# Kernel optimization log

Measured on AMD Instinct MI355X. Metric: run time of the kernel, lower is better.

The kernel has to match this reference:

```python
import jax, jax.numpy as jnp
import numpy as np

N = 20000      # total nodes across the mini-batch of graphs
E = 320000     # edges (avg degree 16)
B = 16         # graphs in the batch
HEADS = 8
EPS_BN = 1e-5
NEG_SLOPE = 0.2


def _lin(k, fan_in, fan_out):
    return (jax.random.normal(k, (fan_in, fan_out), jnp.float32) / np.float32(np.sqrt(fan_in)))


def setup_inputs() -> dict:
    key = jax.random.key(0)
    ks = jax.random.split(key, 24)
    inp = {}
    inp["x"] = jax.random.normal(ks[0], (N, 3), jnp.float32)
    inp["edge_index"] = jax.random.randint(ks[1], (2, E), 0, N, dtype=jnp.int32)
    inp["batch"] = jnp.sort(jax.random.randint(ks[2], (N,), 0, B, dtype=jnp.int32))
    # GATConv params: lin weight [in, heads*out], att_src/att_dst [heads,out], bias [heads*out]
    dims = [(3, 16), (128, 32), (256, 64)]
    for i, (cin, cout) in enumerate(dims, start=1):
        base = 3 + 5 * i
        inp[f"W{i}"] = _lin(ks[base], cin, HEADS * cout)
        inp[f"as{i}"] = jax.random.normal(ks[base + 1], (HEADS, cout), jnp.float32) * 0.1
        inp[f"ad{i}"] = jax.random.normal(ks[base + 2], (HEADS, cout), jnp.float32) * 0.1
        inp[f"b{i}"] = jnp.zeros((HEADS * cout,), jnp.float32)
        inp[f"g{i}"] = jnp.ones((HEADS * cout,), jnp.float32)
        inp[f"be{i}"] = jnp.zeros((HEADS * cout,), jnp.float32)
    inp["fcW"] = _lin(ks[20], 512, 10)
    inp["fcb"] = jnp.zeros((10,), jnp.float32)
    return inp


def gat_layer(x, src, dst, W, a_s, a_d, bias, heads, out_ch):
    n = x.shape[0]
    h = (x @ W).reshape(n, heads, out_ch)              # [N,H,C]
    al_s = jnp.einsum('nhc,hc->nh', h, a_s)            # [N,H]
    al_d = jnp.einsum('nhc,hc->nh', h, a_d)
    e = jax.nn.leaky_relu(al_s[src] + al_d[dst], NEG_SLOPE)   # [E,H]
    m = jax.ops.segment_max(e, dst, num_segments=n)    # per-dst softmax (stable)
    e = jnp.exp(e - m[dst])
    denom = jax.ops.segment_sum(e, dst, num_segments=n)
    alpha = e / (denom[dst] + 1e-16)
    out = jax.ops.segment_sum(h[src] * alpha[:, :, None], dst, num_segments=n)
    return out.reshape(n, heads * out_ch) + bias


def bn_relu(x, g, b):
    mu = x.mean(0)
    var = x.var(0)  # biased, as torch BN uses for normalization
    return jax.nn.relu((x - mu) * jax.lax.rsqrt(var + EPS_BN) * g + b)


def reference(x, edge_index, batch, W1, as1, ad1, b1, g1, be1,
              W2, as2, ad2, b2, g2, be2, W3, as3, ad3, b3, g3, be3, fcW, fcb):
    n = x.shape[0]
    loops = jnp.arange(n, dtype=edge_index.dtype)
    src = jnp.concatenate([edge_index[0], loops])  # add_self_loops=True (PyG default)
    dst = jnp.concatenate([edge_index[1], loops])
    h = bn_relu(gat_layer(x, src, dst, W1, as1, ad1, b1, HEADS, 16), g1, be1)
    h = bn_relu(gat_layer(h, src, dst, W2, as2, ad2, b2, HEADS, 32), g2, be2)
    h = bn_relu(gat_layer(h, src, dst, W3, as3, ad3, b3, HEADS, 64), g3, be3)
    pooled = jax.ops.segment_max(h, batch, num_segments=B)  # global_max_pool
    return pooled @ fcW + fcb
```

## Files before the change

### kernel.cpp

```cpp
#include <hip/hip_runtime.h>
#include <hip/hip_bf16.h>

#define HEADS 8
#define EPS_BN 1e-5f
#define NEG_SLOPE 0.2f
#define BN_NB 256
#define PAD 96

typedef __attribute__((ext_vector_type(8))) short bf16x8;
typedef __attribute__((ext_vector_type(4))) float f32x4;

__device__ __forceinline__ float bf2f(unsigned short u) {
    return __uint_as_float(((unsigned int)u) << 16);
}

__device__ __forceinline__ unsigned short f2bf(float f) {
    __hip_bfloat16 b = __float2bfloat16(f);
    return *reinterpret_cast<unsigned short*>(&b);
}

__device__ __forceinline__ void gld_lds16(const ushort* g, ushort* l) {
    __builtin_amdgcn_global_load_lds(
        (const __attribute__((address_space(1))) unsigned int*)g,
        (__attribute__((address_space(3))) unsigned int*)l, 16, 0, 0);
}


__global__ void scatter_pad_kernel(const int* __restrict__ ei, int E, int N,
                                   int* __restrict__ counts, int* __restrict__ csr_pad) {
    int i = blockIdx.x * blockDim.x + threadIdx.x;
    int total = E + N;
    if (i >= total) return;
    int s, d;
    if (i < E) { s = ei[i]; d = ei[E + i]; } else { s = i - E; d = i - E; }
    int slot = atomicAdd(&counts[d], 1);
    if (slot < PAD) csr_pad[d * PAD + slot] = s;
}


__global__ __launch_bounds__(256) void linear1_al_tr_kernel(const float* __restrict__ x,
                                                            const float* __restrict__ W,
                                                            const float* __restrict__ a_s,
                                                            const float* __restrict__ a_d,
                                                            ushort* __restrict__ h,
                                                            float* __restrict__ als,
                                                            float* __restrict__ ald, int N,
                                                            const float* __restrict__ W2,
                                                            ushort* __restrict__ Wt2,
                                                            const float* __restrict__ W3,
                                                            ushort* __restrict__ Wt3) {
    __shared__ float t[32][33];
    int tid = threadIdx.x;
    int bid = blockIdx.x;
    if (bid < 160) {
        const float* Ws; ushort* Wt; int K, Nc, b;
        if (bid < 32) { Ws = W2; Wt = Wt2; K = 128; Nc = 256; b = bid; }
        else          { Ws = W3; Wt = Wt3; K = 256; Nc = 512; b = bid - 32; }
        int nb = Nc / 32;
        int bx = b % nb, by = b / nb;
        int n0 = bx * 32, k0 = by * 32;
        int lx = tid & 31, ly = tid >> 5;
        for (int r = ly; r < 32; r += 8) t[r][lx] = Ws[(size_t)(k0 + r) * Nc + n0 + lx];
        __syncthreads();
        for (int r = ly; r < 32; r += 8) Wt[(size_t)(n0 + r) * K + k0 + lx] = f2bf(t[lx][r]);
    }
    int n = bid * 2 + (tid >> 7);
    int f = tid & 127;
    if (n >= N) return;
    float acc = x[n * 3 + 0] * W[f] + x[n * 3 + 1] * W[128 + f] + x[n * 3 + 2] * W[256 + f];
    h[(size_t)n * 128 + f] = f2bf(acc);
    float s = acc * a_s[f];
    float ds = acc * a_d[f];
    s += __shfl_xor(s, 1);  ds += __shfl_xor(ds, 1);
    s += __shfl_xor(s, 2);  ds += __shfl_xor(ds, 2);
    s += __shfl_xor(s, 4);  ds += __shfl_xor(ds, 4);
    s += __shfl_xor(s, 8);  ds += __shfl_xor(ds, 8);
    if ((f & 15) == 0) {
        int head = f >> 4;
        als[n * 8 + head] = s;
        ald[n * 8 + head] = ds;
    }
}


template<int K, int C>
__global__ __launch_bounds__(256) void mfma_gemm_kernel(const ushort* __restrict__ A,
                                                        const float* __restrict__ scale,
                                                        const float* __restrict__ shift,
                                                        const ushort* __restrict__ Bt,
                                                        ushort* __restrict__ Cout,
                                                        const float* __restrict__ a_s,
                                                        const float* __restrict__ a_d,
                                                        float* __restrict__ als,
                                                        float* __restrict__ ald,
                                                        int M, int Ncols) {
    __shared__ __align__(16) ushort lA[128 * 64];
    __shared__ __align__(16) ushort lB[128 * 64];
    __shared__ __align__(16) float s_scale[K];
    __shared__ __align__(16) float s_shift[K];
    int tid = threadIdx.x;
    int l = tid & 63, w = tid >> 6;
    int m0 = blockIdx.x * 128;
    int n0 = blockIdx.y * 128;
    int wm = w >> 1, wn = w & 1;
    for (int i = tid; i < K; i += 256) {
        s_scale[i] = scale[i];
        s_shift[i] = shift[i];
    }
    f32x4 zero = {0.f, 0.f, 0.f, 0.f};
    f32x4 acc[4][4];
#pragma unroll
    for (int m = 0; m < 4; ++m)
#pragma unroll
        for (int n = 0; n < 4; ++n) acc[m][n] = zero;
    __syncthreads();

#pragma unroll
    for (int k0 = 0; k0 < K; k0 += 64) {
        if (k0) __syncthreads();
#pragma unroll
        for (int i = 0; i < 4; ++i) {
            int idx = (w * 4 + i) * 64 + l;
            int row = idx >> 3, p = idx & 7;
            int gc = (p ^ (row & 7)) * 8;
            gld_lds16(Bt + (size_t)(n0 + row) * K + k0 + gc, &lB[idx * 8]);
        }
#pragma unroll
        for (int i = 0; i < 4; ++i) {
            int idx = (w * 4 + i) * 64 + l;
            int row = idx >> 3, p = idx & 7;
            int gc = (p ^ (row & 7)) * 8;
            int ar = m0 + row; ar = (ar < M) ? ar : (M - 1);
            int kk = k0 + gc;
            uint4 raw = *(const uint4*)(A + (size_t)ar * K + kk);
            float4 sc0 = *(const float4*)(s_scale + kk);
            float4 sc1 = *(const float4*)(s_scale + kk + 4);
            float4 sh0 = *(const float4*)(s_shift + kk);
            float4 sh1 = *(const float4*)(s_shift + kk + 4);
            unsigned int rr0 = raw.x, rr1 = raw.y, rr2 = raw.z, rr3 = raw.w;
            float v0, v1;
            unsigned int o0, o1, o2, o3;
            v0 = fmaxf(__uint_as_float(rr0 << 16) * sc0.x + sh0.x, 0.f);
            v1 = fmaxf(__uint_as_float(rr0 & 0xffff0000u) * sc0.y + sh0.y, 0.f);
            o0 = (unsigned int)f2bf(v0) | ((unsigned int)f2bf(v1) << 16);
            v0 = fmaxf(__uint_as_float(rr1 << 16) * sc0.z + sh0.z, 0.f);
            v1 = fmaxf(__uint_as_float(rr1 & 0xffff0000u) * sc0.w + sh0.w, 0.f);
            o1 = (unsigned int)f2bf(v0) | ((unsigned int)f2bf(v1) << 16);
            v0 = fmaxf(__uint_as_float(rr2 << 16) * sc1.x + sh1.x, 0.f);
            v1 = fmaxf(__uint_as_float(rr2 & 0xffff0000u) * sc1.y + sh1.y, 0.f);
            o2 = (unsigned int)f2bf(v0) | ((unsigned int)f2bf(v1) << 16);
            v0 = fmaxf(__uint_as_float(rr3 << 16) * sc1.z + sh1.z, 0.f);
            v1 = fmaxf(__uint_as_float(rr3 & 0xffff0000u) * sc1.w + sh1.w, 0.f);
            o3 = (unsigned int)f2bf(v0) | ((unsigned int)f2bf(v1) << 16);
            uint4 pk = {o0, o1, o2, o3};
            *(uint4*)&lA[idx * 8] = pk;
        }
        __syncthreads();
#pragma unroll
        for (int ks = 0; ks < 2; ++ks) {
            bf16x8 af[4], bfr[4];
#pragma unroll
            for (int m = 0; m < 4; ++m) {
                int row = wm * 64 + m * 16 + (l & 15);
                int cp = (ks * 4 + (l >> 4)) ^ (row & 7);
                af[m] = *(const bf16x8*)&lA[row * 64 + cp * 8];
            }
#pragma unroll
            for (int n = 0; n < 4; ++n) {
                int row = wn * 64 + n * 16 + (l & 15);
                int cp = (ks * 4 + (l >> 4)) ^ (row & 7);
                bfr[n] = *(const bf16x8*)&lB[row * 64 + cp * 8];
            }
#pragma unroll
            for (int m = 0; m < 4; ++m)
#pragma unroll
                for (int n = 0; n < 4; ++n)
                    acc[m][n] = __builtin_amdgcn_mfma_f32_16x16x32_bf16(af[m], bfr[n], acc[m][n], 0, 0, 0);
        }
    }
    int lr = (l >> 4) * 4, lc = l & 15;
#pragma unroll
    for (int m = 0; m < 4; ++m) {
#pragma unroll
        for (int q = 0; q < 4; ++q) {
            int r = m0 + wm * 64 + m * 16 + lr + q;
            if (r < M) {
#pragma unroll
                for (int n = 0; n < 4; ++n) {
                    int c = n0 + wn * 64 + n * 16 + lc;
                    Cout[(size_t)r * Ncols + c] = f2bf(acc[m][n][q]);
                }
            }
        }
    }
    constexpr int GRP = (C == 64) ? 4 : 2;
    constexpr int NGRP = 4 / GRP;
    float asv[4], adv[4];
#pragma unroll
    for (int n = 0; n < 4; ++n) {
        int cc = n0 + wn * 64 + n * 16 + lc;
        asv[n] = a_s[cc];
        adv[n] = a_d[cc];
    }
#pragma unroll
    for (int m = 0; m < 4; ++m) {
#pragma unroll
        for (int q = 0; q < 4; ++q) {
            int r = m0 + wm * 64 + m * 16 + lr + q;
#pragma unroll
            for (int gg = 0; gg < NGRP; ++gg) {
                float s = 0.f, ds = 0.f;
#pragma unroll
                for (int nn = 0; nn < GRP; ++nn) {
                    int n = gg * GRP + nn;
                    s += acc[m][n][q] * asv[n];
                    ds += acc[m][n][q] * adv[n];
                }
                s += __shfl_xor(s, 1);  ds += __shfl_xor(ds, 1);
                s += __shfl_xor(s, 2);  ds += __shfl_xor(ds, 2);
                s += __shfl_xor(s, 4);  ds += __shfl_xor(ds, 4);
                s += __shfl_xor(s, 8);  ds += __shfl_xor(ds, 8);
                if (lc == 0 && r < M) {
                    int head = (n0 + wn * 64 + gg * (GRP * 16)) / C;
                    als[r * 8 + head] = s;
                    ald[r * 8 + head] = ds;
                }
            }
        }
    }
}


template<int CPL>
__device__ __forceinline__ void gather_accum(const ushort* hp, float wt, float* acc) {
    unsigned int u[CPL / 2];
    if constexpr (CPL == 8) {
        uint4 v = *(const uint4*)hp; u[0] = v.x; u[1] = v.y; u[2] = v.z; u[3] = v.w;
    } else if constexpr (CPL == 4) {
        uint2 v = *(const uint2*)hp; u[0] = v.x; u[1] = v.y;
    } else {
        u[0] = *(const unsigned int*)hp;
    }
#pragma unroll
    for (int j = 0; j < CPL / 2; ++j) {
        acc[2 * j]     += wt * __uint_as_float(u[j] << 16);
        acc[2 * j + 1] += wt * __uint_as_float(u[j] & 0xffff0000u);
    }
}

template<int F, int C>
__global__ __launch_bounds__(256) void aggregate_kernel(const ushort* __restrict__ h,
                                                        const float* __restrict__ als,
                                                        const float* __restrict__ ald,
                                                        const int* __restrict__ counts,
                                                        const int* __restrict__ csr_pad,
                                                        const float* __restrict__ bias,
                                                        ushort* __restrict__ outbf, int N) {
    constexpr int CPL = F / 64;
    int w = threadIdx.x >> 6, l = threadIdx.x & 63;
    int d = blockIdx.x * 4 + w;
    if (d >= N) return;
    int start = d * PAD;
    int deg = counts[d];
    deg = (deg < PAD) ? deg : PAD;
    int hf = l >> 3;
    int hw = l & 7;
    int jslot = l >> 3;
    float aldw = ald[d * 8 + hw];

    float acc[CPL];
#pragma unroll
    for (int j = 0; j < CPL; ++j) acc[j] = 0.f;
    float dsum = 0.f;
    float mrun = -1e30f;

    int nfull = deg & ~7;
    for (int eb = 0; eb < nfull; eb += 8) {
        int sE = (l < 8) ? csr_pad[start + eb + l] : 0;
        int smy = __shfl(sE, jslot);
        float v = als[smy * 8 + hw] + aldw;
        v = (v > 0.f) ? v : NEG_SLOPE * v;
        float bm = v;
        bm = fmaxf(bm, __shfl_xor(bm, 8));
        bm = fmaxf(bm, __shfl_xor(bm, 16));
        bm = fmaxf(bm, __shfl_xor(bm, 32));
        float mnew = fmaxf(mrun, bm);
        float rs = __expf(mrun - mnew);
        float pw = __expf(v - mnew);
        dsum = dsum * rs + pw;
        float rsg = __shfl(rs, hf);
#pragma unroll
        for (int j = 0; j < CPL; ++j) acc[j] *= rsg;
        mrun = mnew;
#pragma unroll
        for (int j = 0; j < 8; ++j) {
            int sj = __shfl(sE, j);
            float wt = __shfl(pw, (j << 3) + hf);
            gather_accum<CPL>(h + (size_t)sj * F + l * CPL, wt, acc);
        }
    }
    int rem = deg - nfull;
    if (rem) {
        int sE = (l < rem) ? csr_pad[start + nfull + l] : 0;
        int smy = __shfl(sE, jslot);
        float v = -1e30f;
        if (jslot < rem) {
            v = als[smy * 8 + hw] + aldw;
            v = (v > 0.f) ? v : NEG_SLOPE * v;
        }
        float bm = v;
        bm = fmaxf(bm, __shfl_xor(bm, 8));
        bm = fmaxf(bm, __shfl_xor(bm, 16));
        bm = fmaxf(bm, __shfl_xor(bm, 32));
        float mnew = fmaxf(mrun, bm);
        float rs = __expf(mrun - mnew);
        float pw = __expf(v - mnew);
        dsum = dsum * rs + pw;
        float rsg = __shfl(rs, hf);
#pragma unroll
        for (int j = 0; j < CPL; ++j) acc[j] *= rsg;
        for (int j = 0; j < rem; ++j) {
            int sj = __shfl(sE, j);
            float wt = __shfl(pw, (j << 3) + hf);
            gather_accum<CPL>(h + (size_t)sj * F + l * CPL, wt, acc);
        }
    }
    dsum += __shfl_xor(dsum, 8);
    dsum += __shfl_xor(dsum, 16);
    dsum += __shfl_xor(dsum, 32);
    float den = __shfl(dsum, hf);
    float inv = 1.0f / (den + 1e-16f);
    int cbase = l * CPL;
#pragma unroll
    for (int j = 0; j < CPL; ++j)
        outbf[(size_t)d * F + cbase + j] = f2bf(acc[j] * inv + bias[cbase + j]);
}


template<int F>
__global__ __launch_bounds__(256) void bnA_kernel(const ushort* __restrict__ xb,
                                                  float* __restrict__ part,
                                                  int N, int npb) {
    constexpr int F4 = F / 4;
    constexpr int RPI = 256 / F4;
    __shared__ float sdata[256 * 8];
    int tid = threadIdx.x;
    int c4 = tid % F4;
    int ro = tid / F4;
    int n0 = blockIdx.x * npb;
    int n1 = n0 + npb;
    if (n1 > N) n1 = N;
    float s0 = 0, s1 = 0, s2 = 0, s3 = 0, q0 = 0, q1 = 0, q2 = 0, q3 = 0;
    for (int r = n0 + ro; r < n1; r += RPI) {
        ushort4 u = *(const ushort4*)(xb + (size_t)r * F + c4 * 4);
        float v0 = bf2f(u.x), v1 = bf2f(u.y), v2 = bf2f(u.z), v3 = bf2f(u.w);
        s0 += v0; s1 += v1; s2 += v2; s3 += v3;
        q0 += v0 * v0; q1 += v1 * v1; q2 += v2 * v2; q3 += v3 * v3;
    }
    float* sp = &sdata[tid * 8];
    sp[0] = s0; sp[1] = s1; sp[2] = s2; sp[3] = s3;
    sp[4] = q0; sp[5] = q1; sp[6] = q2; sp[7] = q3;
    __syncthreads();
    if (tid < F4) {
        float t[8];
#pragma unroll
        for (int k = 0; k < 8; ++k) t[k] = sdata[tid * 8 + k];
        for (int j = 1; j < RPI; ++j) {
            const float* op = &sdata[(j * F4 + tid) * 8];
#pragma unroll
            for (int k = 0; k < 8; ++k) t[k] += op[k];
        }
        float* pb = part + (size_t)blockIdx.x * 2 * F;
#pragma unroll
        for (int k = 0; k < 4; ++k) {
            pb[tid * 4 + k]     = t[k];
            pb[F + tid * 4 + k] = t[4 + k];
        }
    }
}

template<int F>
__global__ void bnB_kernel(const float* __restrict__ part,
                           const float* __restrict__ g, const float* __restrict__ be,
                           float* __restrict__ scale, float* __restrict__ shift, int N) {
    int f = blockIdx.x * blockDim.x + threadIdx.x;
    if (f >= F) return;
    float sum = 0.f, sq = 0.f;
#pragma unroll 4
    for (int j = 0; j < BN_NB; ++j) {
        sum += part[(size_t)j * 2 * F + f];
        sq  += part[(size_t)j * 2 * F + F + f];
    }
    float invN = 1.0f / (float)N;
    float mean = sum * invN;
    float var = sq * invN - mean * mean;
    float sc = g[f] * rsqrtf(var + EPS_BN);
    scale[f] = sc;
    shift[f] = be[f] - mean * sc;
}


__global__ __launch_bounds__(256) void poolA_kernel(const ushort* __restrict__ xb,
                                                    const int* __restrict__ batch,
                                                    const float* __restrict__ scale,
                                                    const float* __restrict__ shift,
                                                    float* __restrict__ pooled8, int N) {
    int tid = threadIdx.x;
    int c4 = tid & 127;
    int ro = tid >> 7;
    int n0 = blockIdx.x * 64;
    int n1 = n0 + 64;
    if (n1 > N) n1 = N;
    float4 sc = ((const float4*)scale)[c4];
    float4 sh = ((const float4*)shift)[c4];
    float* pbase = pooled8 + (size_t)(blockIdx.x & 7) * (16 * 512);
    float m0 = 0.f, m1 = 0.f, m2 = 0.f, m3 = 0.f;
    int cur = -1;
    for (int n = n0 + ro; n < n1; n += 2) {
        int b = batch[n];
        if (b != cur) {
            if (cur >= 0) {
                int base = cur * 512 + c4 * 4;
                atomicMax((int*)&pbase[base],     __float_as_int(m0));
                atomicMax((int*)&pbase[base + 1], __float_as_int(m1));
                atomicMax((int*)&pbase[base + 2], __float_as_int(m2));
                atomicMax((int*)&pbase[base + 3], __float_as_int(m3));
            }
            cur = b;
            m0 = m1 = m2 = m3 = 0.f;
        }
        ushort4 u = *(const ushort4*)(xb + (size_t)n * 512 + c4 * 4);
        m0 = fmaxf(m0, bf2f(u.x) * sc.x + sh.x);
        m1 = fmaxf(m1, bf2f(u.y) * sc.y + sh.y);
        m2 = fmaxf(m2, bf2f(u.z) * sc.z + sh.z);
        m3 = fmaxf(m3, bf2f(u.w) * sc.w + sh.w);
    }
    if (cur >= 0) {
        int base = cur * 512 + c4 * 4;
        atomicMax((int*)&pbase[base],     __float_as_int(m0));
        atomicMax((int*)&pbase[base + 1], __float_as_int(m1));
        atomicMax((int*)&pbase[base + 2], __float_as_int(m2));
        atomicMax((int*)&pbase[base + 3], __float_as_int(m3));
    }
}

__global__ __launch_bounds__(512) void poolFC_kernel(const float* __restrict__ pooled8,
                                                     const float* __restrict__ fcW,
                                                     const float* __restrict__ fcb,
                                                     float* __restrict__ out) {
    __shared__ float sp[16 * 513];
    __shared__ float sw[512 * 10];
    int tid = threadIdx.x;
    for (int c = tid; c < 16 * 512; c += 512) {
        float m = pooled8[c];
#pragma unroll
        for (int k = 1; k < 8; ++k) m = fmaxf(m, pooled8[k * 16 * 512 + c]);
        int b = c >> 9, f = c & 511;
        sp[b * 513 + f] = m;
    }
    for (int i = tid; i < 512 * 10; i += 512) sw[i] = fcW[i];
    __syncthreads();
    if (tid < 160) {
        int b = tid / 10, j = tid % 10;
        float acc = fcb[j];
        const float* spb = &sp[b * 513];
#pragma unroll 8
        for (int f = 0; f < 512; ++f) acc += spb[f] * sw[f * 10 + j];
        out[tid] = acc;
    }
}


extern "C" void kernel_launch(void* const* d_in, const int* in_sizes, int n_in,
                              void* d_out, int out_size, void* d_ws, size_t ws_size,
                              hipStream_t stream) {
    const float* x   = (const float*)d_in[0];
    const int* ei    = (const int*)d_in[1];
    const int* batch = (const int*)d_in[2];
    const float* W1  = (const float*)d_in[3];
    const float* as1 = (const float*)d_in[4];
    const float* ad1 = (const float*)d_in[5];
    const float* b1  = (const float*)d_in[6];
    const float* g1  = (const float*)d_in[7];
    const float* be1 = (const float*)d_in[8];
    const float* W2  = (const float*)d_in[9];
    const float* as2 = (const float*)d_in[10];
    const float* ad2 = (const float*)d_in[11];
    const float* b2  = (const float*)d_in[12];
    const float* g2  = (const float*)d_in[13];
    const float* be2 = (const float*)d_in[14];
    const float* W3  = (const float*)d_in[15];
    const float* as3 = (const float*)d_in[16];
    const float* ad3 = (const float*)d_in[17];
    const float* b3  = (const float*)d_in[18];
    const float* g3  = (const float*)d_in[19];
    const float* be3 = (const float*)d_in[20];
    const float* fcW = (const float*)d_in[21];
    const float* fcb = (const float*)d_in[22];
    float* out = (float*)d_out;

    int N = in_sizes[0] / 3;
    int E = in_sizes[1] / 2;

    char* p = (char*)d_ws;
    auto alloc = [&](size_t bytes) {
        char* r = p;
        p += (bytes + 255) & ~(size_t)255;
        return r;
    };
    char* zbase   = p;
    int*   counts = (int*)alloc((size_t)N * 4);
    float* pooled8 = (float*)alloc(8 * 16 * 512 * 4);
    size_t zbytes = (size_t)(p - zbase);
    int*   csr_pad = (int*)alloc((size_t)N * PAD * 4);
    ushort* h     = (ushort*)alloc((size_t)N * 512 * 2);
    ushort* aggbf = (ushort*)alloc((size_t)N * 512 * 2);
    ushort* Wt2   = (ushort*)alloc(256 * 128 * 2);
    ushort* Wt3   = (ushort*)alloc(512 * 256 * 2);
    float* als    = (float*)alloc((size_t)N * 8 * 4);
    float* ald    = (float*)alloc((size_t)N * 8 * 4);
    float* bnpart = (float*)alloc((size_t)BN_NB * 1024 * 4);
    float* scale  = (float*)alloc(512 * 4);
    float* shift  = (float*)alloc(512 * 4);

    int total_e = E + N;
    int mtiles = (N + 127) / 128;
    int bnnpb = (N + BN_NB - 1) / BN_NB;
    int ablocks = (N + 3) / 4;
    int pblocks = (N + 63) / 64;

    hipMemsetAsync(zbase, 0, zbytes, stream);

    scatter_pad_kernel<<<(total_e + 255) / 256, 256, 0, stream>>>(ei, E, N, counts, csr_pad);

    linear1_al_tr_kernel<<<(N + 1) / 2, 256, 0, stream>>>(x, W1, as1, ad1, h, als, ald, N,
                                                          W2, Wt2, W3, Wt3);
    aggregate_kernel<128, 16><<<ablocks, 256, 0, stream>>>(h, als, ald, counts, csr_pad, b1, aggbf, N);
    bnA_kernel<128><<<BN_NB, 256, 0, stream>>>(aggbf, bnpart, N, bnnpb);
    bnB_kernel<128><<<1, 128, 0, stream>>>(bnpart, g1, be1, scale, shift, N);

    mfma_gemm_kernel<128, 32><<<dim3(mtiles, 2), 256, 0, stream>>>(
        aggbf, scale, shift, Wt2, h, as2, ad2, als, ald, N, 256);
    aggregate_kernel<256, 32><<<ablocks, 256, 0, stream>>>(h, als, ald, counts, csr_pad, b2, aggbf, N);
    bnA_kernel<256><<<BN_NB, 256, 0, stream>>>(aggbf, bnpart, N, bnnpb);
    bnB_kernel<256><<<1, 256, 0, stream>>>(bnpart, g2, be2, scale, shift, N);

    mfma_gemm_kernel<256, 64><<<dim3(mtiles, 4), 256, 0, stream>>>(
        aggbf, scale, shift, Wt3, h, as3, ad3, als, ald, N, 512);
    aggregate_kernel<512, 64><<<ablocks, 256, 0, stream>>>(h, als, ald, counts, csr_pad, b3, aggbf, N);
    bnA_kernel<512><<<BN_NB, 256, 0, stream>>>(aggbf, bnpart, N, bnnpb);
    bnB_kernel<512><<<2, 256, 0, stream>>>(bnpart, g3, be3, scale, shift, N);

    poolA_kernel<<<pblocks, 256, 0, stream>>>(aggbf, batch, scale, shift, pooled8, N);
    poolFC_kernel<<<1, 512, 0, stream>>>(pooled8, fcW, fcb, out);
}
```

Before: 298.2 us.

## Fuse BN statistics into aggregation and merge scatter with first linear layer

Each aggregate kernel now writes per-block sums and sums of squares of its bf16 outputs through shared memory. That removes the separate bnA pass that re-read the whole aggregated feature matrix. The aggregate block grows to 512 threads (8 destination nodes per block), and bnB is spread over several blocks that reduce the now much larger per-block partial array. The CSR scatter and the layer-1 linear/transpose work are merged into one launch to save a kernel launch. The trade-off is a partial-sum buffer with one row per aggregate block, which bnB must reduce with strided, latency-bound loads from relatively few blocks.

```diff
diff --git a/kernel.cpp b/kernel.cpp
--- a/kernel.cpp
+++ b/kernel.cpp
@@ -4,7 +4,6 @@
 #define HEADS 8
 #define EPS_BN 1e-5f
 #define NEG_SLOPE 0.2f
-#define BN_NB 256
 #define PAD 96
 
 typedef __attribute__((ext_vector_type(8))) short bf16x8;
@@ -26,36 +25,39 @@
 }
 
 
-__global__ void scatter_pad_kernel(const int* __restrict__ ei, int E, int N,
-                                   int* __restrict__ counts, int* __restrict__ csr_pad) {
-    int i = blockIdx.x * blockDim.x + threadIdx.x;
-    int total = E + N;
-    if (i >= total) return;
-    int s, d;
-    if (i < E) { s = ei[i]; d = ei[E + i]; } else { s = i - E; d = i - E; }
-    int slot = atomicAdd(&counts[d], 1);
-    if (slot < PAD) csr_pad[d * PAD + slot] = s;
-}
-
-
-__global__ __launch_bounds__(256) void linear1_al_tr_kernel(const float* __restrict__ x,
-                                                            const float* __restrict__ W,
-                                                            const float* __restrict__ a_s,
-                                                            const float* __restrict__ a_d,
-                                                            ushort* __restrict__ h,
-                                                            float* __restrict__ als,
-                                                            float* __restrict__ ald, int N,
-                                                            const float* __restrict__ W2,
-                                                            ushort* __restrict__ Wt2,
-                                                            const float* __restrict__ W3,
-                                                            ushort* __restrict__ Wt3) {
+__global__ __launch_bounds__(256) void scatter_linear1_kernel(const int* __restrict__ ei, int E,
+                                                              int* __restrict__ counts,
+                                                              int* __restrict__ csr_pad,
+                                                              const float* __restrict__ x,
+                                                              const float* __restrict__ W,
+                                                              const float* __restrict__ a_s,
+                                                              const float* __restrict__ a_d,
+                                                              ushort* __restrict__ h,
+                                                              float* __restrict__ als,
+                                                              float* __restrict__ ald, int N,
+                                                              const float* __restrict__ W2,
+                                                              ushort* __restrict__ Wt2,
+                                                              const float* __restrict__ W3,
+                                                              ushort* __restrict__ Wt3, int nsc) {
     __shared__ float t[32][33];
     int tid = threadIdx.x;
     int bid = blockIdx.x;
-    if (bid < 160) {
+    if (bid < nsc) {
+        int i = bid * 256 + tid;
+        int total = E + N;
+        if (i < total) {
+            int s, d;
+            if (i < E) { s = ei[i]; d = ei[E + i]; } else { s = i - E; d = i - E; }
+            int slot = atomicAdd(&counts[d], 1);
+            if (slot < PAD) csr_pad[d * PAD + slot] = s;
+        }
+        return;
+    }
+    int lb = bid - nsc;
+    if (lb < 160) {
         const float* Ws; ushort* Wt; int K, Nc, b;
-        if (bid < 32) { Ws = W2; Wt = Wt2; K = 128; Nc = 256; b = bid; }
-        else          { Ws = W3; Wt = Wt3; K = 256; Nc = 512; b = bid - 32; }
+        if (lb < 32) { Ws = W2; Wt = Wt2; K = 128; Nc = 256; b = lb; }
+        else         { Ws = W3; Wt = Wt3; K = 256; Nc = 512; b = lb - 32; }
         int nb = Nc / 32;
         int bx = b % nb, by = b / nb;
         int n0 = bx * 32, k0 = by * 32;
@@ -64,7 +66,7 @@
         __syncthreads();
         for (int r = ly; r < 32; r += 8) Wt[(size_t)(n0 + r) * K + k0 + lx] = f2bf(t[lx][r]);
     }
-    int n = bid * 2 + (tid >> 7);
+    int n = lb * 2 + (tid >> 7);
     int f = tid & 127;
     if (n >= N) return;
     float acc = x[n * 3 + 0] * W[f] + x[n * 3 + 1] * W[128 + f] + x[n * 3 + 2] * W[256 + f];
@@ -249,154 +251,151 @@
 }
 
 template<int F, int C>
-__global__ __launch_bounds__(256) void aggregate_kernel(const ushort* __restrict__ h,
+__global__ __launch_bounds__(512) void aggregate_kernel(const ushort* __restrict__ h,
                                                         const float* __restrict__ als,
                                                         const float* __restrict__ ald,
                                                         const int* __restrict__ counts,
                                                         const int* __restrict__ csr_pad,
                                                         const float* __restrict__ bias,
-                                                        ushort* __restrict__ outbf, int N) {
+                                                        ushort* __restrict__ outbf,
+                                                        float* __restrict__ bnpart, int N) {
     constexpr int CPL = F / 64;
-    int w = threadIdx.x >> 6, l = threadIdx.x & 63;
-    int d = blockIdx.x * 4 + w;
-    if (d >= N) return;
-    int start = d * PAD;
-    int deg = counts[d];
-    deg = (deg < PAD) ? deg : PAD;
-    int hf = l >> 3;
-    int hw = l & 7;
-    int jslot = l >> 3;
-    float aldw = ald[d * 8 + hw];
-
-    float acc[CPL];
-#pragma unroll
-    for (int j = 0; j < CPL; ++j) acc[j] = 0.f;
-    float dsum = 0.f;
-    float mrun = -1e30f;
-
-    int nfull = deg & ~7;
-    for (int eb = 0; eb < nfull; eb += 8) {
-        int sE = (l < 8) ? csr_pad[start + eb + l] : 0;
-        int smy = __shfl(sE, jslot);
-        float v = als[smy * 8 + hw] + aldw;
-        v = (v > 0.f) ? v : NEG_SLOPE * v;
-        float bm = v;
-        bm = fmaxf(bm, __shfl_xor(bm, 8));
-        bm = fmaxf(bm, __shfl_xor(bm, 16));
-        bm = fmaxf(bm, __shfl_xor(bm, 32));
-        float mnew = fmaxf(mrun, bm);
-        float rs = __expf(mrun - mnew);
-        float pw = __expf(v - mnew);
-        dsum = dsum * rs + pw;
-        float rsg = __shfl(rs, hf);
-#pragma unroll
-        for (int j = 0; j < CPL; ++j) acc[j] *= rsg;
-        mrun = mnew;
-#pragma unroll
-        for (int j = 0; j < 8; ++j) {
-            int sj = __shfl(sE, j);
-            float wt = __shfl(pw, (j << 3) + hf);
-            gather_accum<CPL>(h + (size_t)sj * F + l * CPL, wt, acc);
-        }
-    }
-    int rem = deg - nfull;
-    if (rem) {
-        int sE = (l < rem) ? csr_pad[start + nfull + l] : 0;
-        int smy = __shfl(sE, jslot);
-        float v = -1e30f;
-        if (jslot < rem) {
-            v = als[smy * 8 + hw] + aldw;
+    __shared__ float sred[8 * 2 * F];
+    int tid = threadIdx.x;
+    int w = tid >> 6, l = tid & 63;
+    int d = blockIdx.x * 8 + w;
+    float* swp = &sred[w * 2 * F];
+    int cbase = l * CPL;
+
+    if (d < N) {
+        int start = d * PAD;
+        int deg = counts[d];
+        deg = (deg < PAD) ? deg : PAD;
+        int hf = l >> 3;
+        int hw = l & 7;
+        int jslot = l >> 3;
+        float aldw = ald[d * 8 + hw];
+
+        float acc[CPL];
+#pragma unroll
+        for (int j = 0; j < CPL; ++j) acc[j] = 0.f;
+        float dsum = 0.f;
+        float mrun = -1e30f;
+
+        int nfull = deg & ~7;
+        for (int eb = 0; eb < nfull; eb += 8) {
+            int sE = (l < 8) ? csr_pad[start + eb + l] : 0;
+            int smy = __shfl(sE, jslot);
+            float v = als[smy * 8 + hw] + aldw;
             v = (v > 0.f) ? v : NEG_SLOPE * v;
-        }
-        float bm = v;
-        bm = fmaxf(bm, __shfl_xor(bm, 8));
-        bm = fmaxf(bm, __shfl_xor(bm, 16));
-        bm = fmaxf(bm, __shfl_xor(bm, 32));
-        float mnew = fmaxf(mrun, bm);
-        float rs = __expf(mrun - mnew);
-        float pw = __expf(v - mnew);
-        dsum = dsum * rs + pw;
-        float rsg = __shfl(rs, hf);
-#pragma unroll
-        for (int j = 0; j < CPL; ++j) acc[j] *= rsg;
-        for (int j = 0; j < rem; ++j) {
-            int sj = __shfl(sE, j);
-            float wt = __shfl(pw, (j << 3) + hf);
-            gather_accum<CPL>(h + (size_t)sj * F + l * CPL, wt, acc);
-        }
-    }
-    dsum += __shfl_xor(dsum, 8);
-    dsum += __shfl_xor(dsum, 16);
-    dsum += __shfl_xor(dsum, 32);
-    float den = __shfl(dsum, hf);
-    float inv = 1.0f / (den + 1e-16f);
-    int cbase = l * CPL;
-#pragma unroll
-    for (int j = 0; j < CPL; ++j)
-        outbf[(size_t)d * F + cbase + j] = f2bf(acc[j] * inv + bias[cbase + j]);
+            float bm = v;
+            bm = fmaxf(bm, __shfl_xor(bm, 8));
+            bm = fmaxf(bm, __shfl_xor(bm, 16));
+            bm = fmaxf(bm, __shfl_xor(bm, 32));
+            float mnew = fmaxf(mrun, bm);
+            float rs = __expf(mrun - mnew);
+            float pw = __expf(v - mnew);
+            dsum = dsum * rs + pw;
+            float rsg = __shfl(rs, hf);
+#pragma unroll
+            for (int j = 0; j < CPL; ++j) acc[j] *= rsg;
+            mrun = mnew;
+#pragma unroll
+            for (int j = 0; j < 8; ++j) {
+                int sj = __shfl(sE, j);
+                float wt = __shfl(pw, (j << 3) + hf);
+                gather_accum<CPL>(h + (size_t)sj * F + l * CPL, wt, acc);
+            }
+        }
+        int rem = deg - nfull;
+        if (rem) {
+            int sE = (l < rem) ? csr_pad[start + nfull + l] : 0;
+            int smy = __shfl(sE, jslot);
+            float v = -1e30f;
+            if (jslot < rem) {
+                v = als[smy * 8 + hw] + aldw;
+                v = (v > 0.f) ? v : NEG_SLOPE * v;
+            }
+            float bm = v;
+            bm = fmaxf(bm, __shfl_xor(bm, 8));
+            bm = fmaxf(bm, __shfl_xor(bm, 16));
+            bm = fmaxf(bm, __shfl_xor(bm, 32));
+            float mnew = fmaxf(mrun, bm);
+            float rs = __expf(mrun - mnew);
+            float pw = __expf(v - mnew);
+            dsum = dsum * rs + pw;
+            float rsg = __shfl(rs, hf);
+#pragma unroll
+            for (int j = 0; j < CPL; ++j) acc[j] *= rsg;
+            for (int j = 0; j < rem; ++j) {
+                int sj = __shfl(sE, j);
+                float wt = __shfl(pw, (j << 3) + hf);
+                gather_accum<CPL>(h + (size_t)sj * F + l * CPL, wt, acc);
+            }
+        }
+        dsum += __shfl_xor(dsum, 8);
+        dsum += __shfl_xor(dsum, 16);
+        dsum += __shfl_xor(dsum, 32);
+        float den = __shfl(dsum, hf);
+        float inv = 1.0f / (den + 1e-16f);
+#pragma unroll
+        for (int j = 0; j < CPL; ++j) {
+            unsigned short ob = f2bf(acc[j] * inv + bias[cbase + j]);
+            outbf[(size_t)d * F + cbase + j] = ob;
+            float vv = bf2f(ob);
+            swp[cbase + j] = vv;
+            swp[F + cbase + j] = vv * vv;
+        }
+    } else {
+#pragma unroll
+        for (int j = 0; j < CPL; ++j) {
+            swp[cbase + j] = 0.f;
+            swp[F + cbase + j] = 0.f;
+        }
+    }
+    __syncthreads();
+    float* pb = bnpart + (size_t)blockIdx.x * 2 * F;
+    for (int i = tid; i < 2 * F; i += 512) {
+        float s = sred[i]           + sred[2 * F + i]  + sred[4 * F + i]  + sred[6 * F + i]
+                + sred[8 * F + i]   + sred[10 * F + i] + sred[12 * F + i] + sred[14 * F + i];
+        pb[i] = s;
+    }
 }
 
 
 template<int F>
-__global__ __launch_bounds__(256) void bnA_kernel(const ushort* __restrict__ xb,
-                                                  float* __restrict__ part,
-                                                  int N, int npb) {
-    constexpr int F4 = F / 4;
-    constexpr int RPI = 256 / F4;
-    __shared__ float sdata[256 * 8];
-    int tid = threadIdx.x;
-    int c4 = tid % F4;
-    int ro = tid / F4;
-    int n0 = blockIdx.x * npb;
-    int n1 = n0 + npb;
-    if (n1 > N) n1 = N;
-    float s0 = 0, s1 = 0, s2 = 0, s3 = 0, q0 = 0, q1 = 0, q2 = 0, q3 = 0;
-    for (int r = n0 + ro; r < n1; r += RPI) {
-        ushort4 u = *(const ushort4*)(xb + (size_t)r * F + c4 * 4);
-        float v0 = bf2f(u.x), v1 = bf2f(u.y), v2 = bf2f(u.z), v3 = bf2f(u.w);
-        s0 += v0; s1 += v1; s2 += v2; s3 += v3;
-        q0 += v0 * v0; q1 += v1 * v1; q2 += v2 * v2; q3 += v3 * v3;
-    }
-    float* sp = &sdata[tid * 8];
-    sp[0] = s0; sp[1] = s1; sp[2] = s2; sp[3] = s3;
-    sp[4] = q0; sp[5] = q1; sp[6] = q2; sp[7] = q3;
+__global__ __launch_bounds__(256) void bnB_kernel(const float* __restrict__ part,
+                                                  const float* __restrict__ g,
+                                                  const float* __restrict__ be,
+                                                  float* __restrict__ scale,
+                                                  float* __restrict__ shift,
+                                                  int N, int nb) {
+    __shared__ float sd[4][64];
+    int t = threadIdx.x;
+    int cl = t & 63;
+    int ro = t >> 6;
+    int fbase = blockIdx.x * 32;
+    size_t coloff = (cl < 32) ? (size_t)(fbase + cl) : (size_t)(F + fbase + (cl - 32));
+    float s = 0.f;
+    for (int j = ro; j < nb; j += 4)
+        s += part[(size_t)j * 2 * F + coloff];
+    sd[ro][cl] = s;
     __syncthreads();
-    if (tid < F4) {
-        float t[8];
-#pragma unroll
-        for (int k = 0; k < 8; ++k) t[k] = sdata[tid * 8 + k];
-        for (int j = 1; j < RPI; ++j) {
-            const float* op = &sdata[(j * F4 + tid) * 8];
-#pragma unroll
-            for (int k = 0; k < 8; ++k) t[k] += op[k];
-        }
-        float* pb = part + (size_t)blockIdx.x * 2 * F;
-#pragma unroll
-        for (int k = 0; k < 4; ++k) {
-            pb[tid * 4 + k]     = t[k];
-            pb[F + tid * 4 + k] = t[4 + k];
-        }
-    }
-}
-
-template<int F>
-__global__ void bnB_kernel(const float* __restrict__ part,
-                           const float* __restrict__ g, const float* __restrict__ be,
-                           float* __restrict__ scale, float* __restrict__ shift, int N) {
-    int f = blockIdx.x * blockDim.x + threadIdx.x;
-    if (f >= F) return;
-    float sum = 0.f, sq = 0.f;
-#pragma unroll 4
-    for (int j = 0; j < BN_NB; ++j) {
-        sum += part[(size_t)j * 2 * F + f];
-        sq  += part[(size_t)j * 2 * F + F + f];
-    }
-    float invN = 1.0f / (float)N;
-    float mean = sum * invN;
-    float var = sq * invN - mean * mean;
-    float sc = g[f] * rsqrtf(var + EPS_BN);
-    scale[f] = sc;
-    shift[f] = be[f] - mean * sc;
+    if (t < 64) {
+        sd[0][t] = sd[0][t] + sd[1][t] + sd[2][t] + sd[3][t];
+    }
+    __syncthreads();
+    if (t < 32) {
+        int f = fbase + t;
+        float sum = sd[0][t];
+        float sq  = sd[0][t + 32];
+        float invN = 1.0f / (float)N;
+        float mean = sum * invN;
+        float var = sq * invN - mean * mean;
+        float sc = g[f] * rsqrtf(var + EPS_BN);
+        scale[f] = sc;
+        shift[f] = be[f] - mean * sc;
+    }
 }
 
 
@@ -519,37 +518,38 @@
     ushort* Wt3   = (ushort*)alloc(512 * 256 * 2);
     float* als    = (float*)alloc((size_t)N * 8 * 4);
     float* ald    = (float*)alloc((size_t)N * 8 * 4);
-    float* bnpart = (float*)alloc((size_t)BN_NB * 1024 * 4);
+    int ablocks   = (N + 7) / 8;
+    float* bnpart = (float*)alloc((size_t)ablocks * 2 * 512 * 4);
     float* scale  = (float*)alloc(512 * 4);
     float* shift  = (float*)alloc(512 * 4);
 
     int total_e = E + N;
+    int nsc = (total_e + 255) / 256;
+    int nlin = (N + 1) / 2;
     int mtiles = (N + 127) / 128;
-    int bnnpb = (N + BN_NB - 1) / BN_NB;
-    int ablocks = (N + 3) / 4;
     int pblocks = (N + 63) / 64;
 
     hipMemsetAsync(zbase, 0, zbytes, stream);
 
-    scatter_pad_kernel<<<(total_e + 255) / 256, 256, 0, stream>>>(ei, E, N, counts, csr_pad);
-
-    linear1_al_tr_kernel<<<(N + 1) / 2, 256, 0, stream>>>(x, W1, as1, ad1, h, als, ald, N,
-                                                          W2, Wt2, W3, Wt3);
-    aggregate_kernel<128, 16><<<ablocks, 256, 0, stream>>>(h, als, ald, counts, csr_pad, b1, aggbf, N);
-    bnA_kernel<128><<<BN_NB, 256, 0, stream>>>(aggbf, bnpart, N, bnnpb);
-    bnB_kernel<128><<<1, 128, 0, stream>>>(bnpart, g1, be1, scale, shift, N);
+    scatter_linear1_kernel<<<nsc + nlin, 256, 0, stream>>>(ei, E, counts, csr_pad,
+                                                           x, W1, as1, ad1, h, als, ald, N,
+                                                           W2, Wt2, W3, Wt3, nsc);
+
+    aggregate_kernel<128, 16><<<ablocks, 512, 0, stream>>>(h, als, ald, counts, csr_pad, b1,
+                                                           aggbf, bnpart, N);
+    bnB_kernel<128><<<4, 256, 0, stream>>>(bnpart, g1, be1, scale, shift, N, ablocks);
 
     mfma_gemm_kernel<128, 32><<<dim3(mtiles, 2), 256, 0, stream>>>(
         aggbf, scale, shift, Wt2, h, as2, ad2, als, ald, N, 256);
-    aggregate_kernel<256, 32><<<ablocks, 256, 0, stream>>>(h, als, ald, counts, csr_pad, b2, aggbf, N);
-    bnA_kernel<256><<<BN_NB, 256, 0, stream>>>(aggbf, bnpart, N, bnnpb);
-    bnB_kernel<256><<<1, 256, 0, stream>>>(bnpart, g2, be2, scale, shift, N);
+    aggregate_kernel<256, 32><<<ablocks, 512, 0, stream>>>(h, als, ald, counts, csr_pad, b2,
+                                                           aggbf, bnpart, N);
+    bnB_kernel<256><<<8, 256, 0, stream>>>(bnpart, g2, be2, scale, shift, N, ablocks);
 
     mfma_gemm_kernel<256, 64><<<dim3(mtiles, 4), 256, 0, stream>>>(
         aggbf, scale, shift, Wt3, h, as3, ad3, als, ald, N, 512);
-    aggregate_kernel<512, 64><<<ablocks, 256, 0, stream>>>(h, als, ald, counts, csr_pad, b3, aggbf, N);
-    bnA_kernel<512><<<BN_NB, 256, 0, stream>>>(aggbf, bnpart, N, bnnpb);
-    bnB_kernel<512><<<2, 256, 0, stream>>>(bnpart, g3, be3, scale, shift, N);
+    aggregate_kernel<512, 64><<<ablocks, 512, 0, stream>>>(h, als, ald, counts, csr_pad, b3,
+                                                           aggbf, bnpart, N);
+    bnB_kernel<512><<<16, 256, 0, stream>>>(bnpart, g3, be3, scale, shift, N, ablocks);
 
     poolA_kernel<<<pblocks, 256, 0, stream>>>(aggbf, batch, scale, shift, pooled8, N);
     poolFC_kernel<<<1, 512, 0, stream>>>(pooled8, fcW, fcb, out);
```

Result: slower. 758.6 us (+154.4%).
